# Kernel optimization log

Hardware: AMD Instinct MI355X
Metric: run time of the kernel (lower is better)

Reference implementation:

```python
import jax, jax.numpy as jnp
import numpy as np

N = 400000      # total atoms across batch of molecules
E = 1600000     # directed edges (avg degree 4)
G = 4096        # number of graphs (molecules)
F_IN = 78       # atomic feature size
H = 128         # gnn hidden dims (gnn_0 = gnn_1 = 128)
FF0, FF1 = 256, 128


def _lin(k, fan_in, fan_out):
    return jax.random.normal(k, (fan_in, fan_out), jnp.float32) / np.sqrt(fan_in).astype(np.float32)


def setup_inputs() -> dict:
    key = jax.random.key(0)
    ks = jax.random.split(key, 10)
    x = jax.random.normal(ks[0], (N, F_IN), jnp.float32)
    edge_index = jax.random.randint(ks[1], (2, E), 0, N, dtype=jnp.int64)
    # sorted graph ids, guaranteed non-empty segments (empty segment -> -inf under max pool)
    batch = (jnp.arange(N, dtype=jnp.int64) * G) // N
    return {
        'x': x, 'edge_index': edge_index, 'batch': batch,
        'W0': _lin(ks[2], F_IN, H), 'b0': jnp.zeros((H,), jnp.float32),
        'W1': _lin(ks[3], H, H),    'b1': jnp.zeros((H,), jnp.float32),
        'Wf0': _lin(ks[4], H, FF0), 'bf0': jnp.zeros((FF0,), jnp.float32),
        'Wf1': _lin(ks[5], FF0, FF1), 'bf1': jnp.zeros((FF1,), jnp.float32),
    }


def _gcn_conv(h, W, b, src, dst, dinv):
    # GCNConv with add_self_loops=True, symmetric normalization.
    hw = h @ W                                     # [N, out]
    norm = dinv[src] * dinv[dst]                   # [E]
    msg = hw[src] * norm[:, None]                  # gather + scale
    agg = jax.ops.segment_sum(msg, dst, num_segments=h.shape[0])
    agg = agg + hw * (dinv * dinv)[:, None]        # self-loop contribution
    return agg + b


def reference(x, edge_index, batch, W0, b0, W1, b1, Wf0, bf0, Wf1, bf1):
    src, dst = edge_index[0], edge_index[1]
    # degree of A + I computed at target nodes (PyG gcn_norm uses col)
    deg = jax.ops.segment_sum(jnp.ones((E,), x.dtype), dst, num_segments=N) + 1.0
    dinv = jax.lax.rsqrt(deg)

    h = jax.nn.relu(_gcn_conv(x, W0, b0, src, dst, dinv))
    h = jax.nn.relu(_gcn_conv(h, W1, b1, src, dst, dinv))

    g = jax.ops.segment_max(h, batch, num_segments=G)   # global max pool [G, H]

    g = jax.nn.relu(g @ Wf0 + bf0)   # dropout is identity in eval
    g = jax.nn.relu(g @ Wf1 + bf1)
    return g
```

## Files before the change

kernel.cpp:

```cpp
#include <hip/hip_runtime.h>
#include <cstdint>
#include <cstddef>

#define NATOMS 400000
#define NEDGES 1600000
#define NGRAPH 4096
#define F_INN  78
#define HDIM   128
#define FF0D   256
#define FF1D   128

#define XPAD   80

typedef __attribute__((ext_vector_type(8))) short short8;
typedef __attribute__((ext_vector_type(4))) short short4v;
typedef __attribute__((ext_vector_type(4))) float f32x4;
typedef __attribute__((ext_vector_type(2))) float f32x2;

static __device__ __forceinline__ short f2bf(float f) {
    unsigned u = __builtin_bit_cast(unsigned, f);
    unsigned r = (u + 0x7fffu + ((u >> 16) & 1u)) >> 16;
    return (short)r;
}
static __device__ __forceinline__ float bf2f(unsigned short u) {
    return __builtin_bit_cast(float, ((unsigned)u) << 16);
}

__global__ __launch_bounds__(256) void k_degi(const int* __restrict__ dst,
                                              int* __restrict__ deg,
                                              int* __restrict__ rank, int E) {
    int e = blockIdx.x * 256 + threadIdx.x;
    if (e < E) rank[e] = atomicAdd(&deg[dst[e]], 1);
}

__global__ __launch_bounds__(256) void k_scan1(int* __restrict__ data,
                                               int* __restrict__ blockSums,
                                               float* __restrict__ dinv, int n) {
    __shared__ int ts[256];
    const int base = blockIdx.x * 1024 + threadIdx.x * 4;
    int v[4];
    #pragma unroll
    for (int j = 0; j < 4; ++j) v[j] = (base + j < n) ? data[base + j] : 0;
    #pragma unroll
    for (int j = 0; j < 4; ++j)
        if (base + j < n) dinv[base + j] = rsqrtf((float)v[j] + 1.0f);
    const int tot = v[0] + v[1] + v[2] + v[3];
    ts[threadIdx.x] = tot;
    __syncthreads();
    #pragma unroll
    for (int off = 1; off < 256; off <<= 1) {
        int t = (threadIdx.x >= off) ? ts[threadIdx.x - off] : 0;
        __syncthreads();
        ts[threadIdx.x] += t;
        __syncthreads();
    }
    int run = ts[threadIdx.x] - tot;
    #pragma unroll
    for (int j = 0; j < 4; ++j) {
        if (base + j < n) data[base + j] = run;
        run += v[j];
    }
    if (threadIdx.x == 255) blockSums[blockIdx.x] = ts[255];
}

__global__ __launch_bounds__(512) void k_scan2(int* __restrict__ blockSums, int nb) {
    __shared__ int ts[512];
    int v = (threadIdx.x < nb) ? blockSums[threadIdx.x] : 0;
    ts[threadIdx.x] = v;
    __syncthreads();
    #pragma unroll
    for (int off = 1; off < 512; off <<= 1) {
        int t = (threadIdx.x >= off) ? ts[threadIdx.x - off] : 0;
        __syncthreads();
        ts[threadIdx.x] += t;
        __syncthreads();
    }
    if (threadIdx.x < nb) blockSums[threadIdx.x] = ts[threadIdx.x] - v;
}

__global__ __launch_bounds__(256) void k_scan3(int* __restrict__ data,
                                               const int* __restrict__ blockSums,
                                               int n, int total) {
    const int off = blockSums[blockIdx.x];
    const int base = blockIdx.x * 1024 + threadIdx.x * 4;
    #pragma unroll
    for (int j = 0; j < 4; ++j)
        if (base + j < n) data[base + j] += off;
    if (blockIdx.x == 0 && threadIdx.x == 0) data[n] = total;
}

__global__ __launch_bounds__(256) void k_fill(const int* __restrict__ src,
                                              const int* __restrict__ dst,
                                              const int* __restrict__ row_start,
                                              const int* __restrict__ rank,
                                              int2* __restrict__ csr_ev,
                                              const float* __restrict__ dinv, int E) {
    int e = blockIdx.x * 256 + threadIdx.x;
    if (e >= E) return;
    int d = dst[e];
    int s = src[e];
    int pos = row_start[d] + rank[e];
    float norm = dinv[s] * dinv[d];
    csr_ev[pos] = make_int2(s, __builtin_bit_cast(int, norm));
}

template<int KC, int KSRC, bool BIASROW>
__global__ __launch_bounds__(64) void k_packw(const float* __restrict__ W,
                                              const float* __restrict__ b,
                                              short* __restrict__ wf) {
    int t = blockIdx.x * 64 + threadIdx.x;
    int f = t >> 6, lane = t & 63;
    int ct = f / KC, kc = f % KC;
    int n  = ct * 16 + (lane & 15);
    int k0 = kc * 32 + (lane >> 4) * 8;
    short8 o;
    #pragma unroll
    for (int j = 0; j < 8; ++j) {
        int k = k0 + j;
        float v = 0.f;
        if (k < KSRC) v = W[(size_t)k * 128 + n];
        else if (BIASROW && k == KSRC) v = b[n];
        o[j] = f2bf(v);
    }
    *(short8*)(wf + (size_t)t * 8) = o;
}

__global__ __launch_bounds__(256) void k_packx(const float* __restrict__ x,
                                               unsigned short* __restrict__ xb) {
    int t = blockIdx.x * 256 + threadIdx.x;
    if (t >= NATOMS * 20) return;
    int n = t / 20, g = t % 20;
    const float* xr = x + (size_t)n * F_INN + g * 4;
    short4v o;
    if (g < 19) {
        f32x2 a = *(const f32x2*)(xr);
        f32x2 b = *(const f32x2*)(xr + 2);
        o.x = f2bf(a.x); o.y = f2bf(a.y); o.z = f2bf(b.x); o.w = f2bf(b.y);
    } else {
        f32x2 a = *(const f32x2*)(xr);
        o.x = f2bf(a.x); o.y = f2bf(a.y); o.z = 0; o.w = 0;
    }
    *(short4v*)(xb + (size_t)n * XPAD + g * 4) = o;
}

__global__ __launch_bounds__(256) void k_gather78(
    const unsigned short* __restrict__ xb, unsigned short* __restrict__ aggx,
    const int* __restrict__ row_start, const int2* __restrict__ csr_ev,
    const float* __restrict__ dinv)
{
    const int n  = blockIdx.x * 32 + (threadIdx.x >> 3);
    const int l  = threadIdx.x & 7;
    const int c8 = l * 8;
    const int ct = 64 + l * 2;
    const float dv = dinv[n];
    const float d2 = dv * dv;

    float acc[8], tacc0, tacc1;
    {
        const short8 sv = *(const short8*)(xb + (size_t)n * XPAD + c8);
        const unsigned tv = *(const unsigned*)(xb + (size_t)n * XPAD + ct);
        #pragma unroll
        for (int j = 0; j < 8; ++j) acc[j] = bf2f((unsigned short)sv[j]) * d2;
        tacc0 = bf2f((unsigned short)(tv & 0xffff)) * d2;
        tacc1 = bf2f((unsigned short)(tv >> 16)) * d2;
    }

    const int s0 = row_start[n], s1 = row_start[n + 1];
    int i = s0;
    for (; i + 3 < s1; i += 4) {
        const int2 e0 = csr_ev[i];
        const int2 e1 = csr_ev[i + 1];
        const int2 e2 = csr_ev[i + 2];
        const int2 e3 = csr_ev[i + 3];
        const short8 r0 = *(const short8*)(xb + (size_t)e0.x * XPAD + c8);
        const short8 r1 = *(const short8*)(xb + (size_t)e1.x * XPAD + c8);
        const short8 r2 = *(const short8*)(xb + (size_t)e2.x * XPAD + c8);
        const short8 r3 = *(const short8*)(xb + (size_t)e3.x * XPAD + c8);
        const unsigned t0 = *(const unsigned*)(xb + (size_t)e0.x * XPAD + ct);
        const unsigned t1 = *(const unsigned*)(xb + (size_t)e1.x * XPAD + ct);
        const unsigned t2 = *(const unsigned*)(xb + (size_t)e2.x * XPAD + ct);
        const unsigned t3 = *(const unsigned*)(xb + (size_t)e3.x * XPAD + ct);
        const float w0 = __builtin_bit_cast(float, e0.y);
        const float w1 = __builtin_bit_cast(float, e1.y);
        const float w2 = __builtin_bit_cast(float, e2.y);
        const float w3 = __builtin_bit_cast(float, e3.y);
        #pragma unroll
        for (int j = 0; j < 8; ++j) acc[j] = fmaf(bf2f((unsigned short)r0[j]), w0, acc[j]);
        #pragma unroll
        for (int j = 0; j < 8; ++j) acc[j] = fmaf(bf2f((unsigned short)r1[j]), w1, acc[j]);
        #pragma unroll
        for (int j = 0; j < 8; ++j) acc[j] = fmaf(bf2f((unsigned short)r2[j]), w2, acc[j]);
        #pragma unroll
        for (int j = 0; j < 8; ++j) acc[j] = fmaf(bf2f((unsigned short)r3[j]), w3, acc[j]);
        tacc0 = fmaf(bf2f((unsigned short)(t0 & 0xffff)), w0, tacc0);
        tacc1 = fmaf(bf2f((unsigned short)(t0 >> 16)),    w0, tacc1);
        tacc0 = fmaf(bf2f((unsigned short)(t1 & 0xffff)), w1, tacc0);
        tacc1 = fmaf(bf2f((unsigned short)(t1 >> 16)),    w1, tacc1);
        tacc0 = fmaf(bf2f((unsigned short)(t2 & 0xffff)), w2, tacc0);
        tacc1 = fmaf(bf2f((unsigned short)(t2 >> 16)),    w2, tacc1);
        tacc0 = fmaf(bf2f((unsigned short)(t3 & 0xffff)), w3, tacc0);
        tacc1 = fmaf(bf2f((unsigned short)(t3 >> 16)),    w3, tacc1);
    }
    for (; i < s1; ++i) {
        const int2 e0 = csr_ev[i];
        const short8 r0 = *(const short8*)(xb + (size_t)e0.x * XPAD + c8);
        const unsigned t0 = *(const unsigned*)(xb + (size_t)e0.x * XPAD + ct);
        const float w0 = __builtin_bit_cast(float, e0.y);
        #pragma unroll
        for (int j = 0; j < 8; ++j) acc[j] = fmaf(bf2f((unsigned short)r0[j]), w0, acc[j]);
        tacc0 = fmaf(bf2f((unsigned short)(t0 & 0xffff)), w0, tacc0);
        tacc1 = fmaf(bf2f((unsigned short)(t0 >> 16)),    w0, tacc1);
    }

    short8 o;
    #pragma unroll
    for (int j = 0; j < 8; ++j) o[j] = f2bf(acc[j]);
    *(short8*)(aggx + (size_t)n * XPAD + c8) = o;
    unsigned to;
    if (l == 7) to = 0x00003F80u;
    else {
        to = (unsigned)(unsigned short)f2bf(tacc0) |
             ((unsigned)(unsigned short)f2bf(tacc1) << 16);
    }
    *(unsigned*)(aggx + (size_t)n * XPAD + ct) = to;
}

template<int KC, int KSRC, bool RELU>
__global__ __launch_bounds__(256) void k_gemm_mfma(
    const short* __restrict__ inv, const short* __restrict__ wfrag,
    short* __restrict__ outp, int M)
{
    constexpr int NFRAG = 8 * KC;
    __shared__ short lds_w[NFRAG * 64 * 8];
    __shared__ __align__(16) char lds_st[4 * 4096];

    const int tid = threadIdx.x;
    #pragma unroll
    for (int it = 0; it < NFRAG * 64 / 256; ++it) {
        int t = it * 256 + tid;
        *(short8*)(lds_w + (size_t)t * 8) = *(const short8*)(wfrag + (size_t)t * 8);
    }
    __syncthreads();

    const int lane = tid & 63;
    const int m = lane & 15, q = lane >> 4;
    const int wid = tid >> 6;
    const int gw = blockIdx.x * 4 + wid;
    const int NW = gridDim.x * 4;
    const int NTILE = M / 16;
    char* const st = lds_st + wid * 4096;

    auto tile_mma = [&](int t, const short8* afr) {
        f32x4 acc[8];
        #pragma unroll
        for (int ct = 0; ct < 8; ++ct) acc[ct] = (f32x4){0.f, 0.f, 0.f, 0.f};
        #pragma unroll
        for (int kc = 0; kc < KC; ++kc)
            #pragma unroll
            for (int ct = 0; ct < 8; ++ct) {
                const short8 wv = *(const short8*)(lds_w + ((size_t)((ct * KC + kc) * 64 + lane)) * 8);
                acc[ct] = __builtin_amdgcn_mfma_f32_16x16x32_bf16(wv, afr[kc], acc[ct], 0, 0, 0);
            }
        #pragma unroll
        for (int ct = 0; ct < 8; ++ct) {
            short4v o;
            float v0 = acc[ct][0], v1 = acc[ct][1], v2 = acc[ct][2], v3 = acc[ct][3];
            if constexpr (RELU) {
                v0 = fmaxf(v0, 0.f); v1 = fmaxf(v1, 0.f);
                v2 = fmaxf(v2, 0.f); v3 = fmaxf(v3, 0.f);
            }
            o.x = f2bf(v0); o.y = f2bf(v1); o.z = f2bf(v2); o.w = f2bf(v3);
            const int c = (ct * 32 + q * 8) ^ ((m & 7) << 4);
            *(short4v*)(st + m * 256 + c) = o;
        }
        #pragma unroll
        for (int p = 0; p < 4; ++p) {
            const int r = p * 4 + (lane >> 4);
            const int c = ((lane & 15) * 16) ^ ((r & 7) << 4);
            const short8 v = *(const short8*)(st + r * 256 + c);
            *(short8*)(outp + (size_t)(t * 16 + r) * 128 + (lane & 15) * 8) = v;
        }
    };

    short8 fA[KC], fB[KC];
    auto load_to = [&](int tile, short8* b) {
        const short* xr = inv + (size_t)(tile * 16 + m) * KSRC;
        #pragma unroll
        for (int kc = 0; kc < KC; ++kc) {
            const int k0 = kc * 32 + q * 8;
            short8 v = {0, 0, 0, 0, 0, 0, 0, 0};
            if (k0 + 8 <= KSRC) v = *(const short8*)(xr + k0);
            b[kc] = v;
        }
    };

    load_to(gw, fA);
    for (int t = gw; t < NTILE; t += NW) {
        const int tn = t + NW;
        if (tn < NTILE) load_to(tn, fB);
        tile_mma(t, fA);
        #pragma unroll
        for (int kc = 0; kc < KC; ++kc) fA[kc] = fB[kc];
    }
}

__global__ __launch_bounds__(256) void k_gather_pool(
    const unsigned short* __restrict__ hw,
    const int* __restrict__ row_start, const int2* __restrict__ csr_ev,
    const float* __restrict__ dinv, const float* __restrict__ bias,
    const int* __restrict__ batch, int* __restrict__ pool, int half)
{
    const int n  = blockIdx.x * 32 + (threadIdx.x >> 3);
    const int c8 = half * 64 + (threadIdx.x & 7) * 8;
    const float dv = dinv[n];
    const float d2 = dv * dv;

    float acc[8];
    {
        const short8 sv = *(const short8*)(hw + (size_t)n * HDIM + c8);
        #pragma unroll
        for (int j = 0; j < 8; ++j)
            acc[j] = fmaf(bf2f((unsigned short)sv[j]), d2, bias[c8 + j]);
    }

    const int s0 = row_start[n], s1 = row_start[n + 1];
    int i = s0;
    for (; i + 3 < s1; i += 4) {
        const int2 e0 = csr_ev[i];
        const int2 e1 = csr_ev[i + 1];
        const int2 e2 = csr_ev[i + 2];
        const int2 e3 = csr_ev[i + 3];
        const short8 r0 = *(const short8*)(hw + (size_t)e0.x * HDIM + c8);
        const short8 r1 = *(const short8*)(hw + (size_t)e1.x * HDIM + c8);
        const short8 r2 = *(const short8*)(hw + (size_t)e2.x * HDIM + c8);
        const short8 r3 = *(const short8*)(hw + (size_t)e3.x * HDIM + c8);
        const float w0 = __builtin_bit_cast(float, e0.y);
        const float w1 = __builtin_bit_cast(float, e1.y);
        const float w2 = __builtin_bit_cast(float, e2.y);
        const float w3 = __builtin_bit_cast(float, e3.y);
        #pragma unroll
        for (int j = 0; j < 8; ++j) acc[j] = fmaf(bf2f((unsigned short)r0[j]), w0, acc[j]);
        #pragma unroll
        for (int j = 0; j < 8; ++j) acc[j] = fmaf(bf2f((unsigned short)r1[j]), w1, acc[j]);
        #pragma unroll
        for (int j = 0; j < 8; ++j) acc[j] = fmaf(bf2f((unsigned short)r2[j]), w2, acc[j]);
        #pragma unroll
        for (int j = 0; j < 8; ++j) acc[j] = fmaf(bf2f((unsigned short)r3[j]), w3, acc[j]);
    }
    for (; i < s1; ++i) {
        const int2 e0 = csr_ev[i];
        const short8 r0 = *(const short8*)(hw + (size_t)e0.x * HDIM + c8);
        const float w0 = __builtin_bit_cast(float, e0.y);
        #pragma unroll
        for (int j = 0; j < 8; ++j) acc[j] = fmaf(bf2f((unsigned short)r0[j]), w0, acc[j]);
    }

    const int gbase = batch[blockIdx.x * 32];
    const int glast = batch[blockIdx.x * 32 + 31];
    const int idx   = batch[n] - gbase;

    float red[2][8];
    #pragma unroll
    for (int s = 0; s < 2; ++s)
        #pragma unroll
        for (int j = 0; j < 8; ++j)
            red[s][j] = (idx == s) ? fmaxf(acc[j], 0.f) : 0.f;

    #pragma unroll
    for (int msk = 8; msk <= 32; msk <<= 1)
        #pragma unroll
        for (int s = 0; s < 2; ++s)
            #pragma unroll
            for (int j = 0; j < 8; ++j)
                red[s][j] = fmaxf(red[s][j], __shfl_xor(red[s][j], msk));

    __shared__ float sm[4][2][64];
    const int wid  = threadIdx.x >> 6;
    const int lane = threadIdx.x & 63;
    if (lane < 8) {
        #pragma unroll
        for (int s = 0; s < 2; ++s)
            #pragma unroll
            for (int j = 0; j < 8; ++j)
                sm[wid][s][lane * 8 + j] = red[s][j];
    }
    __syncthreads();
    if (threadIdx.x < 128) {
        const int s = threadIdx.x >> 6;
        const int f = threadIdx.x & 63;
        if (s == 0 || glast != gbase) {
            float m = fmaxf(fmaxf(sm[0][s][f], sm[1][s][f]),
                            fmaxf(sm[2][s][f], sm[3][s][f]));
            atomicMax(pool + (size_t)(gbase + s) * HDIM + half * 64 + f,
                      __builtin_bit_cast(int, m));
        }
    }
}

template<int K, int NC, bool OUT_RELU_BIAS>
__global__ __launch_bounds__(256) void k_gemm(
    const float* __restrict__ in, const float* __restrict__ W,
    const float* __restrict__ out_bias, float* __restrict__ out0, int M)
{
    constexpr int BK = 32;
    constexpr int TC = NC / 8;
    constexpr int TR = 256 / TC;
    constexpr int ROWS = TR * 8;
    constexpr int XST = ROWS + 4;

    __shared__ float xs[BK][XST];
    __shared__ float ws[BK][NC];

    const int tid = threadIdx.x;
    const int tc  = tid % TC;
    const int tr  = tid / TC;
    const int row0 = blockIdx.x * ROWS;

    float acc[8][8];
    #pragma unroll
    for (int i = 0; i < 8; ++i)
        #pragma unroll
        for (int j = 0; j < 8; ++j) acc[i][j] = 0.f;

    for (int k0 = 0; k0 < K; k0 += BK) {
        {
            constexpr int TASKS = BK * NC / 4;
            #pragma unroll
            for (int it = 0; it < TASKS / 256; ++it) {
                int t  = it * 256 + tid;
                int wk = t / (NC / 4);
                int wc = (t % (NC / 4)) * 4;
                *(float4*)(&ws[wk][wc]) = *(const float4*)(W + (size_t)(k0 + wk) * NC + wc);
            }
        }
        {
            constexpr int TASKS = ROWS * BK / 4;
            #pragma unroll
            for (int it = 0; it < TASKS / 256; ++it) {
                int t   = it * 256 + tid;
                int r   = t / (BK / 4);
                int kq  = (t % (BK / 4)) * 4;
                float4 x4 = *(const float4*)(in + (size_t)(row0 + r) * K + k0 + kq);
                xs[kq + 0][r] = x4.x; xs[kq + 1][r] = x4.y;
                xs[kq + 2][r] = x4.z; xs[kq + 3][r] = x4.w;
            }
        }
        __syncthreads();
        #pragma unroll 8
        for (int kk = 0; kk < BK; ++kk) {
            float a[8], b[8];
            #pragma unroll
            for (int i = 0; i < 8; ++i) a[i] = xs[kk][tr * 8 + i];
            #pragma unroll
            for (int j = 0; j < 8; ++j) b[j] = ws[kk][tc * 8 + j];
            #pragma unroll
            for (int i = 0; i < 8; ++i)
                #pragma unroll
                for (int j = 0; j < 8; ++j)
                    acc[i][j] = fmaf(a[i], b[j], acc[i][j]);
        }
        __syncthreads();
    }

    #pragma unroll
    for (int i = 0; i < 8; ++i) {
        const int row = row0 + tr * 8 + i;
        #pragma unroll
        for (int jq = 0; jq < 2; ++jq) {
            const int col = tc * 8 + jq * 4;
            float4 v;
            v.x = acc[i][jq * 4 + 0]; v.y = acc[i][jq * 4 + 1];
            v.z = acc[i][jq * 4 + 2]; v.w = acc[i][jq * 4 + 3];
            if constexpr (OUT_RELU_BIAS) {
                const float4 bb = *(const float4*)(out_bias + col);
                v.x = fmaxf(v.x + bb.x, 0.f); v.y = fmaxf(v.y + bb.y, 0.f);
                v.z = fmaxf(v.z + bb.z, 0.f); v.w = fmaxf(v.w + bb.w, 0.f);
            }
            *(float4*)(out0 + (size_t)row * NC + col) = v;
        }
    }
}

extern "C" void kernel_launch(void* const* d_in, const int* in_sizes, int n_in,
                              void* d_out, int out_size, void* d_ws, size_t ws_size,
                              hipStream_t stream) {
    const float* x    = (const float*)d_in[0];
    const int*   ei   = (const int*)d_in[1];
    const int*   batch= (const int*)d_in[2];
    const float* W0   = (const float*)d_in[3];
    const float* b0   = (const float*)d_in[4];
    const float* W1   = (const float*)d_in[5];
    const float* b1   = (const float*)d_in[6];
    const float* Wf0  = (const float*)d_in[7];
    const float* bf0  = (const float*)d_in[8];
    const float* Wf1  = (const float*)d_in[9];
    const float* bf1  = (const float*)d_in[10];
    float* out = (float*)d_out;

    const int* srcI = ei;
    const int* dstI = ei + NEDGES;

    constexpr int SCAN_NBLK = (NATOMS + 1023) / 1024;

    char* base = (char*)d_ws;
    unsigned short* hwA  = (unsigned short*)(base + 0);
    unsigned short* aggx = (unsigned short*)(base + 0);
    unsigned short* aggB = (unsigned short*)(base + 102400000);
    unsigned short* xb   = (unsigned short*)(base + 102400000);
    int*   rank      = (int*)(base + 102400000);
    float* dinv      = (float*)(base + 204800000);
    int*   row_start = (int*)(base + 206400000);
    int2*  csr_ev    = (int2*)(base + 208000064);
    int*   blockSums = (int*)(base + 220800064);
    float* pool      = (float*)(base + 220802112);
    float* ff0       = (float*)(base + 222899264);
    short* wf0       = (short*)(base + 227093568);
    short* wf1       = (short*)(base + 227118144);

    hipMemsetAsync(row_start, 0, (size_t)(NATOMS + 1) * sizeof(int), stream);
    hipMemsetAsync(pool, 0, (size_t)NGRAPH * HDIM * sizeof(float), stream);
    k_degi<<<(NEDGES + 255) / 256, 256, 0, stream>>>(dstI, row_start, rank, NEDGES);
    k_scan1<<<SCAN_NBLK, 256, 0, stream>>>(row_start, blockSums, dinv, NATOMS);
    k_scan2<<<1, 512, 0, stream>>>(blockSums, SCAN_NBLK);
    k_scan3<<<SCAN_NBLK, 256, 0, stream>>>(row_start, blockSums, NATOMS, NEDGES);
    k_fill<<<(NEDGES + 255) / 256, 256, 0, stream>>>(srcI, dstI, row_start, rank,
                                                     csr_ev, dinv, NEDGES);

    k_packw<3, F_INN, true><<<8 * 3, 64, 0, stream>>>(W0, b0, wf0);
    k_packw<4, HDIM, false><<<8 * 4, 64, 0, stream>>>(W1, nullptr, wf1);
    k_packx<<<(NATOMS * 20 + 255) / 256, 256, 0, stream>>>(x, xb);

    k_gather78<<<NATOMS / 32, 256, 0, stream>>>(xb, aggx, row_start, csr_ev, dinv);
    k_gemm_mfma<3, XPAD, true><<<1024, 256, 0, stream>>>((const short*)aggx, wf0,
                                                         (short*)aggB, NATOMS);

    k_gemm_mfma<4, HDIM, false><<<1024, 256, 0, stream>>>((const short*)aggB, wf1,
                                                          (short*)hwA, NATOMS);
    k_gather_pool<<<NATOMS / 32, 256, 0, stream>>>(hwA, row_start, csr_ev,
                                                   dinv, b1, batch, (int*)pool, 0);
    k_gather_pool<<<NATOMS / 32, 256, 0, stream>>>(hwA, row_start, csr_ev,
                                                   dinv, b1, batch, (int*)pool, 1);

    k_gemm<HDIM, FF0D, true><<<NGRAPH / 64, 256, 0, stream>>>(pool, Wf0, bf0, ff0, NGRAPH);
    k_gemm<FF0D, FF1D, true><<<NGRAPH / 128, 256, 0, stream>>>(ff0, Wf1, bf1, out, NGRAPH);
}
```

Baseline: 650.1 us.

## Fuse layer-0 neighbor gather with MFMA GEMM via shared memory staging

Merges the layer-0 aggregation kernel and the following bf16 MFMA GEMM into one kernel. Each block aggregates 32 nodes into LDS, then multiplies them by the packed W0 fragments and writes ReLU'd bf16 output directly. This removes the global write and re-read of the aggregated 80-wide features plus one launch. In exchange every one of the 12500 blocks reloads the 24KB weight fragment set, and the larger LDS footprint may reduce occupancy for the latency-bound gather. The workspace is relaid so xb no longer aliases the output buffer.

```diff
diff --git a/kernel.cpp b/kernel.cpp
--- a/kernel.cpp
+++ b/kernel.cpp
@@ -143,86 +143,145 @@
     *(short4v*)(xb + (size_t)n * XPAD + g * 4) = o;
 }
 
-__global__ __launch_bounds__(256) void k_gather78(
-    const unsigned short* __restrict__ xb, unsigned short* __restrict__ aggx,
+__global__ __launch_bounds__(256) void k_fused0(
+    const unsigned short* __restrict__ xb, const short* __restrict__ wfrag,
     const int* __restrict__ row_start, const int2* __restrict__ csr_ev,
-    const float* __restrict__ dinv)
+    const float* __restrict__ dinv, short* __restrict__ outp)
 {
-    const int n  = blockIdx.x * 32 + (threadIdx.x >> 3);
-    const int l  = threadIdx.x & 7;
-    const int c8 = l * 8;
-    const int ct = 64 + l * 2;
-    const float dv = dinv[n];
-    const float d2 = dv * dv;
-
-    float acc[8], tacc0, tacc1;
+    constexpr int XLDS = 104;
+    __shared__ short lds_w[24 * 64 * 8];
+    __shared__ __align__(16) unsigned short xs[32 * XLDS];
+    __shared__ __align__(16) char lds_st[4 * 2048];
+
+    const int tid = threadIdx.x;
+    #pragma unroll
+    for (int it = 0; it < 6; ++it) {
+        int t = it * 256 + tid;
+        *(short8*)(lds_w + (size_t)t * 8) = *(const short8*)(wfrag + (size_t)t * 8);
+    }
+
     {
-        const short8 sv = *(const short8*)(xb + (size_t)n * XPAD + c8);
-        const unsigned tv = *(const unsigned*)(xb + (size_t)n * XPAD + ct);
-        #pragma unroll
-        for (int j = 0; j < 8; ++j) acc[j] = bf2f((unsigned short)sv[j]) * d2;
-        tacc0 = bf2f((unsigned short)(tv & 0xffff)) * d2;
-        tacc1 = bf2f((unsigned short)(tv >> 16)) * d2;
-    }
-
-    const int s0 = row_start[n], s1 = row_start[n + 1];
-    int i = s0;
-    for (; i + 3 < s1; i += 4) {
-        const int2 e0 = csr_ev[i];
-        const int2 e1 = csr_ev[i + 1];
-        const int2 e2 = csr_ev[i + 2];
-        const int2 e3 = csr_ev[i + 3];
-        const short8 r0 = *(const short8*)(xb + (size_t)e0.x * XPAD + c8);
-        const short8 r1 = *(const short8*)(xb + (size_t)e1.x * XPAD + c8);
-        const short8 r2 = *(const short8*)(xb + (size_t)e2.x * XPAD + c8);
-        const short8 r3 = *(const short8*)(xb + (size_t)e3.x * XPAD + c8);
-        const unsigned t0 = *(const unsigned*)(xb + (size_t)e0.x * XPAD + ct);
-        const unsigned t1 = *(const unsigned*)(xb + (size_t)e1.x * XPAD + ct);
-        const unsigned t2 = *(const unsigned*)(xb + (size_t)e2.x * XPAD + ct);
-        const unsigned t3 = *(const unsigned*)(xb + (size_t)e3.x * XPAD + ct);
-        const float w0 = __builtin_bit_cast(float, e0.y);
-        const float w1 = __builtin_bit_cast(float, e1.y);
-        const float w2 = __builtin_bit_cast(float, e2.y);
-        const float w3 = __builtin_bit_cast(float, e3.y);
-        #pragma unroll
-        for (int j = 0; j < 8; ++j) acc[j] = fmaf(bf2f((unsigned short)r0[j]), w0, acc[j]);
-        #pragma unroll
-        for (int j = 0; j < 8; ++j) acc[j] = fmaf(bf2f((unsigned short)r1[j]), w1, acc[j]);
-        #pragma unroll
-        for (int j = 0; j < 8; ++j) acc[j] = fmaf(bf2f((unsigned short)r2[j]), w2, acc[j]);
-        #pragma unroll
-        for (int j = 0; j < 8; ++j) acc[j] = fmaf(bf2f((unsigned short)r3[j]), w3, acc[j]);
-        tacc0 = fmaf(bf2f((unsigned short)(t0 & 0xffff)), w0, tacc0);
-        tacc1 = fmaf(bf2f((unsigned short)(t0 >> 16)),    w0, tacc1);
-        tacc0 = fmaf(bf2f((unsigned short)(t1 & 0xffff)), w1, tacc0);
-        tacc1 = fmaf(bf2f((unsigned short)(t1 >> 16)),    w1, tacc1);
-        tacc0 = fmaf(bf2f((unsigned short)(t2 & 0xffff)), w2, tacc0);
-        tacc1 = fmaf(bf2f((unsigned short)(t2 >> 16)),    w2, tacc1);
-        tacc0 = fmaf(bf2f((unsigned short)(t3 & 0xffff)), w3, tacc0);
-        tacc1 = fmaf(bf2f((unsigned short)(t3 >> 16)),    w3, tacc1);
-    }
-    for (; i < s1; ++i) {
-        const int2 e0 = csr_ev[i];
-        const short8 r0 = *(const short8*)(xb + (size_t)e0.x * XPAD + c8);
-        const unsigned t0 = *(const unsigned*)(xb + (size_t)e0.x * XPAD + ct);
-        const float w0 = __builtin_bit_cast(float, e0.y);
-        #pragma unroll
-        for (int j = 0; j < 8; ++j) acc[j] = fmaf(bf2f((unsigned short)r0[j]), w0, acc[j]);
-        tacc0 = fmaf(bf2f((unsigned short)(t0 & 0xffff)), w0, tacc0);
-        tacc1 = fmaf(bf2f((unsigned short)(t0 >> 16)),    w0, tacc1);
-    }
-
-    short8 o;
-    #pragma unroll
-    for (int j = 0; j < 8; ++j) o[j] = f2bf(acc[j]);
-    *(short8*)(aggx + (size_t)n * XPAD + c8) = o;
-    unsigned to;
-    if (l == 7) to = 0x00003F80u;
-    else {
-        to = (unsigned)(unsigned short)f2bf(tacc0) |
-             ((unsigned)(unsigned short)f2bf(tacc1) << 16);
-    }
-    *(unsigned*)(aggx + (size_t)n * XPAD + ct) = to;
+        const int nl = tid >> 3;
+        const int n  = blockIdx.x * 32 + nl;
+        const int l  = tid & 7;
+        const int c8 = l * 8;
+        const int ct = 64 + l * 2;
+        const float dv = dinv[n];
+        const float d2 = dv * dv;
+
+        float acc[8], tacc0, tacc1;
+        {
+            const short8 sv = *(const short8*)(xb + (size_t)n * XPAD + c8);
+            const unsigned tv = *(const unsigned*)(xb + (size_t)n * XPAD + ct);
+            #pragma unroll
+            for (int j = 0; j < 8; ++j) acc[j] = bf2f((unsigned short)sv[j]) * d2;
+            tacc0 = bf2f((unsigned short)(tv & 0xffff)) * d2;
+            tacc1 = bf2f((unsigned short)(tv >> 16)) * d2;
+        }
+
+        const int s0 = row_start[n], s1 = row_start[n + 1];
+        int i = s0;
+        for (; i + 3 < s1; i += 4) {
+            const int2 e0 = csr_ev[i];
+            const int2 e1 = csr_ev[i + 1];
+            const int2 e2 = csr_ev[i + 2];
+            const int2 e3 = csr_ev[i + 3];
+            const short8 r0 = *(const short8*)(xb + (size_t)e0.x * XPAD + c8);
+            const short8 r1 = *(const short8*)(xb + (size_t)e1.x * XPAD + c8);
+            const short8 r2 = *(const short8*)(xb + (size_t)e2.x * XPAD + c8);
+            const short8 r3 = *(const short8*)(xb + (size_t)e3.x * XPAD + c8);
+            const unsigned t0 = *(const unsigned*)(xb + (size_t)e0.x * XPAD + ct);
+            const unsigned t1 = *(const unsigned*)(xb + (size_t)e1.x * XPAD + ct);
+            const unsigned t2 = *(const unsigned*)(xb + (size_t)e2.x * XPAD + ct);
+            const unsigned t3 = *(const unsigned*)(xb + (size_t)e3.x * XPAD + ct);
+            const float w0 = __builtin_bit_cast(float, e0.y);
+            const float w1 = __builtin_bit_cast(float, e1.y);
+            const float w2 = __builtin_bit_cast(float, e2.y);
+            const float w3 = __builtin_bit_cast(float, e3.y);
+            #pragma unroll
+            for (int j = 0; j < 8; ++j) acc[j] = fmaf(bf2f((unsigned short)r0[j]), w0, acc[j]);
+            #pragma unroll
+            for (int j = 0; j < 8; ++j) acc[j] = fmaf(bf2f((unsigned short)r1[j]), w1, acc[j]);
+            #pragma unroll
+            for (int j = 0; j < 8; ++j) acc[j] = fmaf(bf2f((unsigned short)r2[j]), w2, acc[j]);
+            #pragma unroll
+            for (int j = 0; j < 8; ++j) acc[j] = fmaf(bf2f((unsigned short)r3[j]), w3, acc[j]);
+            tacc0 = fmaf(bf2f((unsigned short)(t0 & 0xffff)), w0, tacc0);
+            tacc1 = fmaf(bf2f((unsigned short)(t0 >> 16)),    w0, tacc1);
+            tacc0 = fmaf(bf2f((unsigned short)(t1 & 0xffff)), w1, tacc0);
+            tacc1 = fmaf(bf2f((unsigned short)(t1 >> 16)),    w1, tacc1);
+            tacc0 = fmaf(bf2f((unsigned short)(t2 & 0xffff)), w2, tacc0);
+            tacc1 = fmaf(bf2f((unsigned short)(t2 >> 16)),    w2, tacc1);
+            tacc0 = fmaf(bf2f((unsigned short)(t3 & 0xffff)), w3, tacc0);
+            tacc1 = fmaf(bf2f((unsigned short)(t3 >> 16)),    w3, tacc1);
+        }
+        for (; i < s1; ++i) {
+            const int2 e0 = csr_ev[i];
+            const short8 r0 = *(const short8*)(xb + (size_t)e0.x * XPAD + c8);
+            const unsigned t0 = *(const unsigned*)(xb + (size_t)e0.x * XPAD + ct);
+            const float w0 = __builtin_bit_cast(float, e0.y);
+            #pragma unroll
+            for (int j = 0; j < 8; ++j) acc[j] = fmaf(bf2f((unsigned short)r0[j]), w0, acc[j]);
+            tacc0 = fmaf(bf2f((unsigned short)(t0 & 0xffff)), w0, tacc0);
+            tacc1 = fmaf(bf2f((unsigned short)(t0 >> 16)),    w0, tacc1);
+        }
+
+        short8 o;
+        #pragma unroll
+        for (int j = 0; j < 8; ++j) o[j] = f2bf(acc[j]);
+        *(short8*)(xs + nl * XLDS + c8) = o;
+        unsigned to;
+        if (l == 7) to = 0x00003F80u;
+        else {
+            to = (unsigned)(unsigned short)f2bf(tacc0) |
+                 ((unsigned)(unsigned short)f2bf(tacc1) << 16);
+        }
+        *(unsigned*)(xs + nl * XLDS + ct) = to;
+        *(unsigned*)(xs + nl * XLDS + 80 + l * 2) = 0u;
+    }
+    __syncthreads();
+
+    const int lane = tid & 63;
+    const int wid  = tid >> 6;
+    const int m = lane & 15, q = lane >> 4;
+    const int T  = wid >> 1;
+    const int c0 = (wid & 1) * 4;
+
+    short8 afr[3];
+    #pragma unroll
+    for (int kc = 0; kc < 3; ++kc)
+        afr[kc] = *(const short8*)(xs + (T * 16 + m) * XLDS + kc * 32 + q * 8);
+
+    f32x4 acc[4];
+    #pragma unroll
+    for (int cc = 0; cc < 4; ++cc) acc[cc] = (f32x4){0.f, 0.f, 0.f, 0.f};
+    #pragma unroll
+    for (int kc = 0; kc < 3; ++kc)
+        #pragma unroll
+        for (int cc = 0; cc < 4; ++cc) {
+            const short8 wv = *(const short8*)(lds_w + ((size_t)(((c0 + cc) * 3 + kc) * 64 + lane)) * 8);
+            acc[cc] = __builtin_amdgcn_mfma_f32_16x16x32_bf16(wv, afr[kc], acc[cc], 0, 0, 0);
+        }
+
+    char* const st = lds_st + wid * 2048;
+    #pragma unroll
+    for (int cc = 0; cc < 4; ++cc) {
+        short4v o;
+        o.x = f2bf(fmaxf(acc[cc][0], 0.f));
+        o.y = f2bf(fmaxf(acc[cc][1], 0.f));
+        o.z = f2bf(fmaxf(acc[cc][2], 0.f));
+        o.w = f2bf(fmaxf(acc[cc][3], 0.f));
+        const int c = (cc * 32 + q * 8) ^ ((m & 7) << 4);
+        *(short4v*)(st + m * 128 + c) = o;
+    }
+    #pragma unroll
+    for (int p = 0; p < 2; ++p) {
+        const int r  = p * 8 + (lane >> 3);
+        const int cb = ((lane & 7) * 16) ^ ((r & 7) << 4);
+        const short8 v = *(const short8*)(st + r * 128 + cb);
+        *(short8*)(outp + (size_t)(blockIdx.x * 32 + T * 16 + r) * 128
+                        + c0 * 16 + (lane & 7) * 8) = v;
+    }
 }
 
 template<int KC, int KSRC, bool RELU>
@@ -504,10 +563,8 @@
 
     char* base = (char*)d_ws;
     unsigned short* hwA  = (unsigned short*)(base + 0);
-    unsigned short* aggx = (unsigned short*)(base + 0);
+    int*   rank      = (int*)(base + 0);
     unsigned short* aggB = (unsigned short*)(base + 102400000);
-    unsigned short* xb   = (unsigned short*)(base + 102400000);
-    int*   rank      = (int*)(base + 102400000);
     float* dinv      = (float*)(base + 204800000);
     int*   row_start = (int*)(base + 206400000);
     int2*  csr_ev    = (int2*)(base + 208000064);
@@ -516,6 +573,7 @@
     float* ff0       = (float*)(base + 222899264);
     short* wf0       = (short*)(base + 227093568);
     short* wf1       = (short*)(base + 227118144);
+    unsigned short* xb = (unsigned short*)(base + 227150912);
 
     hipMemsetAsync(row_start, 0, (size_t)(NATOMS + 1) * sizeof(int), stream);
     hipMemsetAsync(pool, 0, (size_t)NGRAPH * HDIM * sizeof(float), stream);
@@ -530,9 +588,8 @@
     k_packw<4, HDIM, false><<<8 * 4, 64, 0, stream>>>(W1, nullptr, wf1);
     k_packx<<<(NATOMS * 20 + 255) / 256, 256, 0, stream>>>(x, xb);
 
-    k_gather78<<<NATOMS / 32, 256, 0, stream>>>(xb, aggx, row_start, csr_ev, dinv);
-    k_gemm_mfma<3, XPAD, true><<<1024, 256, 0, stream>>>((const short*)aggx, wf0,
-                                                         (short*)aggB, NATOMS);
+    k_fused0<<<NATOMS / 32, 256, 0, stream>>>(xb, wf0, row_start, csr_ev, dinv,
+                                              (short*)aggB);
 
     k_gemm_mfma<4, HDIM, false><<<1024, 256, 0, stream>>>((const short*)aggB, wf1,
                                                           (short*)hwA, NATOMS);
```

Result: no change. 658.1 us (+1.2%).
